# Kernel optimization log

Hardware: AMD Instinct MI355X
Metric: run time of the kernel (lower is better)

## Reference

```python
import jax, jax.numpy as jnp
import numpy as np

B, S, D, MULT, K, EPS = 8, 2048, 512, 4, 9, 1e-6


def setup_inputs() -> dict:
    key = jax.random.key(0)
    ks = jax.random.split(key, 12)
    w = lambda k, shape, s=0.02: jax.random.normal(k, shape, dtype=jnp.float32) * s
    return dict(
        x=jax.random.normal(ks[0], (B, S, D), dtype=jnp.float32),
        g=jnp.ones((D,), jnp.float32),
        W1=w(ks[1], (D, D)), b1=jnp.zeros((D,), jnp.float32),
        W2=w(ks[2], (D, D)), b2=jnp.zeros((D,), jnp.float32),
        dw_w=w(ks[3], (D, D, K)), dw_b=jnp.zeros((D,), jnp.float32),
        pw_w=w(ks[4], (D, D, 1)), pw_b=jnp.zeros((D,), jnp.float32),
        Wi=w(ks[5], (D, D)), bi=jnp.zeros((D,), jnp.float32),
        Wr=w(ks[6], (D, D)), br=jnp.zeros((D,), jnp.float32),
        lam=jax.random.normal(ks[7], (D,), dtype=jnp.float32),
        Wm1=w(ks[8], (D, D * MULT)), bm1=jnp.zeros((D * MULT,), jnp.float32),
        Wm2=w(ks[9], (D * MULT, D)), bm2=jnp.zeros((D,), jnp.float32),
    )


def _rglru(x, Wi, bi, Wr, br, lam):
    # Griffin RG-LRU: h_t = a_t * h_{t-1} + sqrt(1 - a_t^2) * (i_t * x_t), h_0 = 0
    r = jax.nn.sigmoid(x @ Wr + br)                 # [B,S,D] recurrence gate
    i = jax.nn.sigmoid(x @ Wi + bi)                 # [B,S,D] input gate
    log_a = -8.0 * jax.nn.softplus(lam) * r         # [B,S,D]
    a = jnp.exp(log_a)
    b = jnp.sqrt(1.0 - jnp.exp(2.0 * log_a)) * (i * x)

    def combine(e1, e2):
        a1, b1 = e1
        a2, b2 = e2
        return (a1 * a2, a2 * b1 + b2)

    _, h = jax.lax.associative_scan(combine, (a, b), axis=1)
    return h


def _conv1d(x_cdS, w_oik, b_o, pad):
    y = jax.lax.conv_general_dilated(
        x_cdS, w_oik, window_strides=(1,), padding=[pad],
        dimension_numbers=("NCH", "OIH", "NCH"))
    return y + b_o[None, :, None]


def reference(x, g, W1, b1, W2, b2, dw_w, dw_b, pw_w, pw_b,
              Wi, bi, Wr, br, lam, Wm1, bm1, Wm2, bm2):
    scale = jnp.sqrt(jnp.float32(D))

    def rms(t):  # matches torch: x / (||x||_2 + eps) * sqrt(D) * g
        n = jnp.linalg.norm(t, axis=-1, keepdims=True) + EPS
        return t / n * scale * g

    skip = x
    xn = rms(x)
    l1 = xn @ W1 + b1                               # [B,S,D]
    l2 = xn @ W2 + b2                               # [B,S,D]
    c = jnp.transpose(l1, (0, 2, 1))                # [B,D,S]
    c = _conv1d(c, dw_w, dw_b, (K // 2, K // 2))    # 'same' padding, k=9
    c = _conv1d(c, pw_w, pw_b, (0, 0))              # pointwise k=1
    l1 = jnp.transpose(c, (0, 2, 1))                # [B,S,D]
    l1 = _rglru(l1, Wi, bi, Wr, br, lam)
    x1 = l1 * jax.nn.gelu(l2, approximate=False) + skip

    skip2 = x1
    xn2 = rms(x1)
    h = xn2 @ Wm1 + bm1                             # [B,S,4D]
    out = (jax.nn.gelu(h, approximate=False) * h) @ Wm2 + bm2 + skip2
    return out
```

## Files before the change

kernel.cpp:

```cpp
#include <hip/hip_runtime.h>
#include <hip/hip_bf16.h>

typedef unsigned short ushort_t;
typedef unsigned short vus8 __attribute__((ext_vector_type(8)));
typedef short vs8 __attribute__((ext_vector_type(8)));
typedef float vf4 __attribute__((ext_vector_type(4)));

#define D_DIM 512
#define S_LEN 2048
#define B_SZ 8
#define T_TOK 16384
#define NCH 64
#define CLEN 32
#define APAD_ROWS 16640

__device__ __forceinline__ float bf2f(ushort_t u) {
  union { unsigned int i; float f; } v;
  v.i = ((unsigned int)u) << 16;
  return v.f;
}
__device__ __forceinline__ ushort_t f2bf(float f) {
  union { float f; unsigned int i; } v;
  v.f = f;
  unsigned int r = v.i + 0x7fffu + ((v.i >> 16) & 1u);
  return (ushort_t)(r >> 16);
}
__device__ __forceinline__ float gelu_exact(float x) {
  return 0.5f * x * (1.0f + erff(x * 0.7071067811865475f));
}
__device__ __forceinline__ float ld_in(const void* p, size_t i, int fl) {
  return fl ? ((const float*)p)[i] : bf2f(((const ushort_t*)p)[i]);
}
__device__ __forceinline__ int dt_fl(const ushort_t* gdt) {
  return !(gdt[0] == 0x3F80 && gdt[1] == 0x3F80);
}
__device__ __forceinline__ void gld_lds16(const ushort_t* g, ushort_t* l) {
  __builtin_amdgcn_global_load_lds(
      (const __attribute__((address_space(1))) unsigned int*)g,
      (__attribute__((address_space(3))) unsigned int*)l, 16, 0, 0);
}

__device__ __forceinline__ void ab_compute(ushort_t rp, ushort_t ip, ushort_t xv,
                                           float sp8, float& a, float& b) {
  float r = 1.f / (1.f + expf(-bf2f(rp)));
  float ig = 1.f / (1.f + expf(-bf2f(ip)));
  float la = -sp8 * r;
  a = expf(la);
  b = sqrtf(fmaxf(0.f, -expm1f(2.f * la))) * ig * bf2f(xv);
}

#define NJOBS 27
struct PrepJobs {
  const void* src[NJOBS];
  ushort_t* dst[NJOBS];
  int R[NJOBS];
  int C[NJOBS];
  int mode[NJOBS];
  int start[NJOBS];
  const void* gsrc;
  int njobs;
};
__global__ void mega_prep(PrepJobs J, const ushort_t* __restrict__ gdt) {
  __shared__ ushort_t ts[32][33];
  int fl = dt_fl(gdt);
  int bid = blockIdx.x;
  int j = 0;
  while (j + 1 < J.njobs && bid >= J.start[j + 1]) j++;
  int tile = bid - J.start[j];
  const void* in = J.src[j];
  ushort_t* out = J.dst[j];
  int mode = J.mode[j];
  if (mode == 2 || mode == 4) {
    int n = J.R[j];
    int base = tile * 8192;
#pragma unroll 4
    for (int q = 0; q < 32; q++) {
      int i = base + q * 256 + threadIdx.x;
      if (i < n)
        out[i] = (mode == 4) ? (ushort_t)0
                             : (fl ? f2bf(((const float*)in)[i]) : ((const ushort_t*)in)[i]);
    }
    return;
  }
  int R = J.R[j], C = J.C[j];
  int tpr = C >> 5;
  int bc = tile % tpr, br = tile / tpr;
  int tx = threadIdx.x & 31, ty = threadIdx.x >> 5;
#pragma unroll
  for (int i = 0; i < 32; i += 8) {
    size_t idx = (size_t)(br * 32 + ty + i) * C + bc * 32 + tx;
    ts[ty + i][tx] = fl ? f2bf(((const float*)in)[idx]) : ((const ushort_t*)in)[idx];
  }
  __syncthreads();
#pragma unroll
  for (int i = 0; i < 32; i += 8) {
    int r = bc * 32 + ty + i;
    int orow = (mode == 1) ? (r % 9) * 512 + r / 9 : r;
    ushort_t val = ts[tx][ty + i];
    if (mode == 3) {
      int kcol = br * 32 + tx;
      val = f2bf(bf2f(val) * ld_in(J.gsrc, kcol, fl));
    }
    out[(size_t)orow * R + br * 32 + tx] = val;
  }
}

__global__ void gam_kernel(const ushort_t* __restrict__ tpw, const ushort_t* __restrict__ dwbc,
                           const ushort_t* __restrict__ pwbc, const ushort_t* __restrict__ lamc,
                           float* __restrict__ gam, float* __restrict__ sp8b) {
  int t = blockIdx.x * 256 + threadIdx.x;
  if (t < 512) {
    float l = bf2f(lamc[t]);
    sp8b[t] = 8.f * ((l > 20.f) ? l : log1pf(expf(l)));
  }
  int wave = threadIdx.x >> 6, lane = threadIdx.x & 63;
  int o = blockIdx.x * 4 + wave;
  vus8 v = *(const vus8*)(tpw + (size_t)o * 512 + lane * 8);
  vus8 w = *(const vus8*)(dwbc + lane * 8);
  float p = 0.f;
#pragma unroll
  for (int q = 0; q < 8; q++) p += bf2f(v[q]) * bf2f(w[q]);
#pragma unroll
  for (int off = 32; off; off >>= 1) p += __shfl_xor(p, off, 64);
  if (lane == 0) gam[o] = p + bf2f(pwbc[o]);
}

__global__ void rms_kernel(const void* __restrict__ x, const ushort_t* __restrict__ gdt,
                           const ushort_t* __restrict__ gc, ushort_t* __restrict__ out) {
  int fl = dt_fl(gdt);
  int wave = threadIdx.x >> 6, lane = threadIdx.x & 63;
  int row = blockIdx.x * 4 + wave;
  size_t base = (size_t)row * D_DIM + lane * 8;
  float f[8];
  float ss = 0.f;
#pragma unroll
  for (int j = 0; j < 8; j++) { f[j] = ld_in(x, base + j, fl); ss += f[j] * f[j]; }
#pragma unroll
  for (int off = 32; off > 0; off >>= 1) ss += __shfl_xor(ss, off, 64);
  float sc = 22.62741699796952f / (sqrtf(ss) + 1e-6f);
  vus8 o;
#pragma unroll
  for (int j = 0; j < 8; j++) o[j] = f2bf(f[j] * sc * bf2f(gc[lane * 8 + j]));
  *(vus8*)(out + base) = o;
}

template <int ACT>
__global__ __launch_bounds__(256, 2) void gemm_bt(
    const ushort_t* __restrict__ A, const ushort_t* __restrict__ Bt,
    const ushort_t* __restrict__ bias, void* __restrict__ Cv,
    const ushort_t* __restrict__ skip, const float* __restrict__ rowss,
    const ushort_t* __restrict__ gdt, int N, int K, int lda, int row0,
    size_t zsA, size_t zsB, size_t zsC) {
  __shared__ __align__(16) ushort_t As[128 * 32];
  __shared__ __align__(16) ushort_t Bs[128 * 32];
  A += (size_t)blockIdx.z * zsA;
  Bt += (size_t)blockIdx.z * zsB;
  const size_t zC = (size_t)blockIdx.z * zsC;
  const int tid = threadIdx.x;
  const int bm = blockIdx.y, bn = blockIdx.x;
  const int wave = tid >> 6, lane = tid & 63;
  const int wm = wave & 1, wn = wave >> 1;
  const int quad = lane >> 4, l16 = lane & 15;
  const int ofl = (ACT == 2) ? dt_fl(gdt) : 0;
  const int srow = wave * 32 + (lane >> 2);
  const int scol = (lane & 3) * 8;
  const ushort_t* gA = A + (size_t)(bm * 128 + srow) * lda + scol;
  const ushort_t* gB = Bt + (size_t)(bn * 128 + srow) * K + scol;
  ushort_t* lA0 = As + (wave * 32) * 32;
  ushort_t* lA1 = As + (wave * 32 + 16) * 32;
  ushort_t* lB0 = Bs + (wave * 32) * 32;
  ushort_t* lB1 = Bs + (wave * 32 + 16) * 32;
  vf4 acc[4][4] = {};
  for (int k0 = 0; k0 < K; k0 += 32) {
    __syncthreads();
    gld_lds16(gA + k0, lA0);
    gld_lds16(gA + k0 + (size_t)16 * lda, lA1);
    gld_lds16(gB + k0, lB0);
    gld_lds16(gB + k0 + (size_t)16 * K, lB1);
    __syncthreads();
    vs8 af[4], bfr[4];
#pragma unroll
    for (int mi = 0; mi < 4; mi++)
      af[mi] = *(const vs8*)(As + (wm * 64 + mi * 16 + l16) * 32 + quad * 8);
#pragma unroll
    for (int ni = 0; ni < 4; ni++)
      bfr[ni] = *(const vs8*)(Bs + (wn * 64 + ni * 16 + l16) * 32 + quad * 8);
#pragma unroll
    for (int mi = 0; mi < 4; mi++)
#pragma unroll
      for (int ni = 0; ni < 4; ni++)
        acc[mi][ni] =
            __builtin_amdgcn_mfma_f32_16x16x32_bf16(af[mi], bfr[ni], acc[mi][ni], 0, 0, 0);
  }
#pragma unroll
  for (int mi = 0; mi < 4; mi++) {
#pragma unroll
    for (int ni = 0; ni < 4; ni++) {
      int gcol = bn * 128 + wn * 64 + ni * 16 + l16;
      float bv = bias ? bf2f(bias[gcol]) : 0.f;
#pragma unroll
      for (int r = 0; r < 4; r++) {
        int grow = row0 + bm * 128 + wm * 64 + mi * 16 + quad * 4 + r;
        size_t oidx = zC + (size_t)grow * N + gcol;
        float v;
        if (ACT == 3) {
          float sc = 22.62741699796952f / (sqrtf(rowss[grow]) + 1e-6f);
          v = acc[mi][ni][r] * sc + bv;
          v = gelu_exact(v) * v;
        } else {
          v = acc[mi][ni][r] + bv;
        }
        if (ACT == 2) v += bf2f(skip[(size_t)grow * N + gcol]);
        if (ACT == 2 && ofl) ((float*)Cv)[oidx] = v;
        else ((ushort_t*)Cv)[oidx] = f2bf(v);
      }
    }
  }
}

template <int ACT>
__global__ __launch_bounds__(512, 2) void gemm256(
    const ushort_t* __restrict__ A, const ushort_t* __restrict__ Bt,
    const ushort_t* __restrict__ bias, ushort_t* __restrict__ C,
    const float* __restrict__ rowss, int N, int K) {
  __shared__ __align__(16) ushort_t lds[65536];
  const int tid = threadIdx.x;
  const int bn = blockIdx.x, bm = blockIdx.y;
  const int wave = tid >> 6, lane = tid & 63;
  const int wm = wave & 1, wn = wave >> 1;
  const int quad = lane >> 4, l16 = lane & 15;
  const int NT = K >> 5;

  const int r2 = tid >> 2;
  const int scol = (((tid & 3) ^ ((r2 >> 1) & 3)) << 3);
  const ushort_t* gA0 = A + (size_t)(bm * 256 + r2) * K + scol;
  const ushort_t* gB0 = Bt + (size_t)(bn * 256 + r2) * K + scol;
  const size_t hstep = (size_t)128 * K;
  ushort_t* ldsW = lds + (wave << 9);

  const int cA = ((quad ^ ((l16 >> 1) & 3)) << 3);

  vf4 acc[8][4] = {};

#define STAGE(t, slot)                            \
  do {                                            \
    const ushort_t* ga = gA0 + (t) * 32;          \
    const ushort_t* gb = gB0 + (t) * 32;          \
    ushort_t* d = ldsW + (slot) * 16384;          \
    gld_lds16(ga, d);                             \
    gld_lds16(ga + hstep, d + 4096);              \
    gld_lds16(gb, d + 8192);                      \
    gld_lds16(gb + hstep, d + 12288);             \
  } while (0)

  STAGE(0, 0);
  STAGE(1, 1);

  for (int t = 0; t < NT; ++t) {
    if (t + 1 < NT)
      asm volatile("s_waitcnt vmcnt(4)" ::: "memory");
    else
      asm volatile("s_waitcnt vmcnt(0)" ::: "memory");
    __builtin_amdgcn_s_barrier();
    __builtin_amdgcn_sched_barrier(0);
    if (t + 2 < NT) STAGE(t + 2, (t + 2) & 3);
    const ushort_t* L = lds + (t & 3) * 16384;
    vs8 af[8], bf[4];
#pragma unroll
    for (int mi = 0; mi < 8; mi++)
      af[mi] = *(const vs8*)(L + (wm * 128 + mi * 16 + l16) * 32 + cA);
#pragma unroll
    for (int ni = 0; ni < 4; ni++)
      bf[ni] = *(const vs8*)(L + 8192 + (wn * 64 + ni * 16 + l16) * 32 + cA);
    asm volatile("s_waitcnt lgkmcnt(0)" ::: "memory");
    __builtin_amdgcn_sched_barrier(0);
    __builtin_amdgcn_s_setprio(1);
#pragma unroll
    for (int mi = 0; mi < 8; mi++)
#pragma unroll
      for (int ni = 0; ni < 4; ni++)
        acc[mi][ni] =
            __builtin_amdgcn_mfma_f32_16x16x32_bf16(af[mi], bf[ni], acc[mi][ni], 0, 0, 0);
    __builtin_amdgcn_s_setprio(0);
    __builtin_amdgcn_sched_barrier(0);
  }
#undef STAGE

#pragma unroll
  for (int mi = 0; mi < 8; mi++) {
    const int growb = bm * 256 + wm * 128 + mi * 16 + quad * 4;
    float scv[4];
    if (ACT == 3) {
#pragma unroll
      for (int r = 0; r < 4; r++)
        scv[r] = 22.62741699796952f / (sqrtf(rowss[growb + r]) + 1e-6f);
    }
#pragma unroll
    for (int ni = 0; ni < 4; ni++) {
      const int gcol = bn * 256 + wn * 64 + ni * 16 + l16;
      const float bv = bf2f(bias[gcol]);
#pragma unroll
      for (int r = 0; r < 4; r++) {
        float v = acc[mi][ni][r];
        if (ACT == 3) {
          v = v * scv[r] + bv;
          v = gelu_exact(v) * v;
        } else {
          v += bv;
        }
        int grow = growb + r;
        size_t orow = (ACT == 1) ? (size_t)grow + (size_t)((grow >> 11) << 4) + 4
                                 : (size_t)grow;
        C[orow * N + gcol] = f2bf(v);
      }
    }
  }
}

__global__ __launch_bounds__(512, 2) void conv256(
    const ushort_t* __restrict__ Apad, const ushort_t* __restrict__ Wp,
    const float* __restrict__ gam, ushort_t* __restrict__ C) {
  __shared__ __align__(16) ushort_t Asl[2 * 12288];
  __shared__ __align__(16) ushort_t Bsl[4 * 4096];
  const int tid = threadIdx.x;
  const int bn = blockIdx.x;
  const int bmg = blockIdx.y;
  const int batch = bmg >> 3, seg = bmg & 7;
  const int wave = tid >> 6, lane = tid & 63;
  const int wm = wave >> 1, wn = wave & 1;
  const int quad = lane >> 4, l16 = lane & 15;
  const int r2 = tid >> 2;
  const int sw0 = (((tid & 3) ^ ((r2 >> 1) & 3)) << 3);
  const int cB = ((quad ^ ((l16 >> 1) & 3)) << 3);
  const int bnc = bn * 128;
  const size_t tb = (size_t)batch * 2064 + seg * 256;
  const ushort_t* A0 = Apad + tb * 1024;

  vf4 acc[4][4] = {};

  auto stageA = [&](int tt, int slot, int part) {
    gld_lds16(A0 + (size_t)(part * 128 + r2) * 1024 + tt * 32 + sw0,
              Asl + slot * 12288 + part * 4096 + wave * 512);
  };
  auto stageB = [&](int tt, int pp, int slot) {
    gld_lds16(Wp + (size_t)(pp * 512 + bnc + r2) * 512 + tt * 32 + sw0,
              Bsl + slot * 4096 + wave * 512);
  };

#define CPHASE(T, P, NSTR, DO_A, DO_B)                                            \
  do {                                                                            \
    asm volatile("s_waitcnt " NSTR ::: "memory");                                 \
    __builtin_amdgcn_s_barrier();                                                 \
    __builtin_amdgcn_sched_barrier(0);                                            \
    if (DO_A) stageA((T) + 1, ((T) + 1) & 1, (P));                                \
    if (DO_B) {                                                                   \
      int pp = (P) + 2, tt = (T);                                                 \
      if (pp >= 9) { pp -= 9; tt++; }                                             \
      stageB(tt, pp, ((T) * 9 + (P) + 2) & 3);                                    \
    }                                                                             \
    const ushort_t* LA = Asl + ((T) & 1) * 12288;                                 \
    const ushort_t* LB = Bsl + (((T) * 9 + (P)) & 3) * 4096;                      \
    vs8 af[4], bfv[4];                                                            \
    _Pragma("unroll") for (int mi = 0; mi < 4; mi++) {                            \
      int row = wm * 64 + mi * 16 + l16 + (P);                                    \
      af[mi] = *(const vs8*)(LA + row * 32 + ((quad ^ ((row >> 1) & 3)) << 3));   \
    }                                                                             \
    _Pragma("unroll") for (int ni = 0; ni < 4; ni++)                              \
      bfv[ni] = *(const vs8*)(LB + (wn * 64 + ni * 16 + l16) * 32 + cB);          \
    asm volatile("s_waitcnt lgkmcnt(0)" ::: "memory");                            \
    __builtin_amdgcn_sched_barrier(0);                                            \
    __builtin_amdgcn_s_setprio(1);                                                \
    _Pragma("unroll") for (int mi = 0; mi < 4; mi++)                              \
      _Pragma("unroll") for (int ni = 0; ni < 4; ni++)                            \
        acc[mi][ni] = __builtin_amdgcn_mfma_f32_16x16x32_bf16(af[mi], bfv[ni],    \
                                                              acc[mi][ni], 0, 0, 0); \
    __builtin_amdgcn_s_setprio(0);                                                \
    __builtin_amdgcn_sched_barrier(0);                                            \
  } while (0)

  stageA(0, 0, 0);
  stageA(0, 0, 1);
  stageA(0, 0, 2);
  stageB(0, 0, 0);
  stageB(0, 1, 1);

  for (int t = 0; t < 15; ++t) {
    CPHASE(t, 0, "vmcnt(1)", 1, 1);
    CPHASE(t, 1, "vmcnt(2)", 1, 1);
    CPHASE(t, 2, "vmcnt(2)", 1, 1);
    CPHASE(t, 3, "vmcnt(2)", 0, 1);
    CPHASE(t, 4, "vmcnt(1)", 0, 1);
    CPHASE(t, 5, "vmcnt(1)", 0, 1);
    CPHASE(t, 6, "vmcnt(1)", 0, 1);
    CPHASE(t, 7, "vmcnt(1)", 0, 1);
    CPHASE(t, 8, "vmcnt(1)", 0, 1);
  }
  {
    const int t = 15;
    CPHASE(t, 0, "vmcnt(0)", 0, 1);
    CPHASE(t, 1, "vmcnt(0)", 0, 1);
    CPHASE(t, 2, "vmcnt(0)", 0, 1);
    CPHASE(t, 3, "vmcnt(0)", 0, 1);
    CPHASE(t, 4, "vmcnt(0)", 0, 1);
    CPHASE(t, 5, "vmcnt(0)", 0, 1);
    CPHASE(t, 6, "vmcnt(0)", 0, 1);
    CPHASE(t, 7, "vmcnt(0)", 0, 0);
    CPHASE(t, 8, "vmcnt(0)", 0, 0);
  }
#undef CPHASE

#pragma unroll
  for (int mi = 0; mi < 4; mi++) {
#pragma unroll
    for (int ni = 0; ni < 4; ni++) {
      int gcol = bnc + wn * 64 + ni * 16 + l16;
      float gv = gam[gcol];
#pragma unroll
      for (int r = 0; r < 4; r++) {
        int grow = (batch << 11) + seg * 256 + wm * 64 + mi * 16 + quad * 4 + r;
        C[(size_t)grow * D_DIM + gcol] = f2bf(acc[mi][ni][r] + gv);
      }
    }
  }
}

__global__ void scan_pass1(const ushort_t* __restrict__ P, const ushort_t* __restrict__ xin,
                           const float* __restrict__ sp8b, float* __restrict__ Aagg,
                           float* __restrict__ Bagg) {
  int bid = blockIdx.x;
  int dblk = bid & 1, c = (bid >> 1) & (NCH - 1), bb = bid >> 7;
  int d = dblk * 256 + threadIdx.x;
  float sp8 = sp8b[d];
  size_t baseP = ((size_t)bb * S_LEN + c * CLEN) * 1024 + d;
  size_t baseX = ((size_t)bb * S_LEN + c * CLEN) * D_DIM + d;
  float Ap = 1.f, h = 0.f;
  for (int s = 0; s < CLEN; s++) {
    float av, bv;
    ab_compute(P[baseP + (size_t)s * 1024], P[baseP + 512 + (size_t)s * 1024],
               xin[baseX + (size_t)s * D_DIM], sp8, av, bv);
    Ap *= av;
    h = av * h + bv;
  }
  size_t o = ((size_t)bb * NCH + c) * D_DIM + d;
  Aagg[o] = Ap;
  Bagg[o] = h;
}

__global__ void scan_carry(const float* __restrict__ Aagg, const float* __restrict__ Bagg,
                           float* __restrict__ carry) {
  int idx = blockIdx.x * 256 + threadIdx.x;
  int bb = idx >> 9, d = idx & (D_DIM - 1);
  float h = 0.f;
  for (int c = 0; c < NCH; c++) {
    size_t o = ((size_t)bb * NCH + c) * D_DIM + d;
    carry[o] = h;
    h = Aagg[o] * h + Bagg[o];
  }
}

__global__ void scan_pass2(const ushort_t* __restrict__ P, const float* __restrict__ sp8b,
                           const float* __restrict__ carry, const ushort_t* __restrict__ l2p,
                           const void* __restrict__ x, const ushort_t* __restrict__ gdt,
                           ushort_t* xio, float* __restrict__ rowss) {
  int fl = dt_fl(gdt);
  int bid = blockIdx.x;
  int dblk = bid & 1, c = (bid >> 1) & (NCH - 1), bb = bid >> 7;
  int d = dblk * 256 + threadIdx.x;
  int lane = threadIdx.x & 63;
  float sp8 = sp8b[d];
  float h = carry[((size_t)bb * NCH + c) * D_DIM + d];
  size_t baseP = ((size_t)bb * S_LEN + c * CLEN) * 1024 + d;
  size_t baseL = ((size_t)bb * 2064 + 4 + c * CLEN) * 1024 + 512 + d;
  size_t base = ((size_t)bb * S_LEN + c * CLEN) * D_DIM + d;
  int row0 = bb * S_LEN + c * CLEN;
  for (int s = 0; s < CLEN; s++) {
    size_t idx = base + (size_t)s * D_DIM;
    float av, bv;
    ab_compute(P[baseP + (size_t)s * 1024], P[baseP + 512 + (size_t)s * 1024], xio[idx], sp8,
               av, bv);
    h = av * h + bv;
    float l2v = bf2f(l2p[baseL + (size_t)s * 1024]);
    float xv = ld_in(x, idx, fl);
    float v = h * gelu_exact(l2v) + xv;
    xio[idx] = f2bf(v);
    float p = v * v;
#pragma unroll
    for (int o2 = 32; o2; o2 >>= 1) p += __shfl_xor(p, o2, 64);
    if (lane == 0) atomicAdd(&rowss[row0 + s], p);
  }
}

extern "C" void kernel_launch(void* const* d_in, const int* in_sizes, int n_in, void* d_out,
                              int out_size, void* d_ws, size_t ws_size, hipStream_t stream) {
  (void)in_sizes; (void)n_in; (void)out_size; (void)ws_size;
  const void* x   = d_in[0];
  const void* g   = d_in[1];
  const void* W1  = d_in[2];
  const void* b1  = d_in[3];
  const void* W2  = d_in[4];
  const void* b2  = d_in[5];
  const void* dww = d_in[6];
  const void* dwb = d_in[7];
  const void* pww = d_in[8];
  const void* pwb = d_in[9];
  const void* Wi  = d_in[10];
  const void* bi  = d_in[11];
  const void* Wr  = d_in[12];
  const void* br  = d_in[13];
  const void* lam = d_in[14];
  const void* Wm1 = d_in[15];
  const void* bm1 = d_in[16];
  const void* Wm2 = d_in[17];
  const void* bm2 = d_in[18];
  const ushort_t* gdt = (const ushort_t*)g;

  char* ws = (char*)d_ws;
  size_t off = 0;
  auto take = [&](size_t n) {
    void* p = ws + off;
    off += (n + 255) & ~(size_t)255;
    return p;
  };
  const size_t ACT_B = (size_t)T_TOK * D_DIM * 2;
  ushort_t* tW12 = (ushort_t*)take((size_t)1024 * 512 * 2);
  ushort_t* tWri = (ushort_t*)take((size_t)1024 * 512 * 2);
  ushort_t* tWm1 = (ushort_t*)take((size_t)2048 * 512 * 2);
  ushort_t* tWm2 = (ushort_t*)take((size_t)2048 * 512 * 2);
  ushort_t* Wp   = (ushort_t*)take((size_t)9 * 512 * 512 * 2);
  ushort_t* gc   = (ushort_t*)take(512 * 2);
  ushort_t* lamc = (ushort_t*)take(512 * 2);
  ushort_t* b12c = (ushort_t*)take(1024 * 2);
  ushort_t* bric = (ushort_t*)take(1024 * 2);
  ushort_t* bm2c = (ushort_t*)take(512 * 2);
  ushort_t* bm1c = (ushort_t*)take(2048 * 2);
  ushort_t* dwbc = (ushort_t*)take(512 * 2);
  ushort_t* pwbc = (ushort_t*)take(512 * 2);
  float* gam     = (float*)take(512 * 4);
  float* sp8b    = (float*)take(512 * 4);
  float* rowss   = (float*)take((size_t)T_TOK * 4);
  ushort_t* Apad2 = (ushort_t*)take((size_t)APAD_ROWS * 1024 * 2);
  ushort_t* PriB  = (ushort_t*)take((size_t)T_TOK * 1024 * 2);
  ushort_t* S4    = (ushort_t*)take(ACT_B);
  float* Aagg  = (float*)take((size_t)B_SZ * NCH * D_DIM * 4);
  float* Bagg  = (float*)take((size_t)B_SZ * NCH * D_DIM * 4);
  float* carry = (float*)take((size_t)B_SZ * NCH * D_DIM * 4);
  ushort_t* tpw  = PriB;
  ushort_t* tdwT = PriB + 262144;
  ushort_t* u    = Apad2;

  hipMemsetAsync(rowss, 0, (size_t)T_TOK * 4, stream);

  PrepJobs J;
  const void* js[NJOBS] = {g, lam, b1, b2, dwb, pwb, br, bi, bm2, bm1, pww,
                           W1, W2, Wr, Wi, Wm1, Wm2, dww,
                           nullptr, nullptr, nullptr, nullptr, nullptr, nullptr, nullptr,
                           nullptr, nullptr};
  ushort_t* jd[NJOBS] = {gc, lamc, b12c, b12c + 512, dwbc, pwbc, bric, bric + 512, bm2c, bm1c,
                         tpw, tW12, tW12 + (size_t)512 * 512, tWri, tWri + (size_t)512 * 512,
                         tWm1, tWm2, tdwT,
                         Apad2,
                         Apad2 + (size_t)(0 * 2064 + 2052) * 1024,
                         Apad2 + (size_t)(1 * 2064 + 2052) * 1024,
                         Apad2 + (size_t)(2 * 2064 + 2052) * 1024,
                         Apad2 + (size_t)(3 * 2064 + 2052) * 1024,
                         Apad2 + (size_t)(4 * 2064 + 2052) * 1024,
                         Apad2 + (size_t)(5 * 2064 + 2052) * 1024,
                         Apad2 + (size_t)(6 * 2064 + 2052) * 1024,
                         Apad2 + (size_t)(7 * 2064 + 2052) * 1024};
  int jR[NJOBS] = {512, 512, 512, 512, 512, 512, 512, 512, 512, 2048, 262144,
                   512, 512, 512, 512, 512, 2048, 512,
                   4096, 16384, 16384, 16384, 16384, 16384, 16384, 16384, 12288};
  int jC[NJOBS] = {0, 0, 0, 0, 0, 0, 0, 0, 0, 0, 0, 512, 512, 512, 512, 2048, 512, 4608,
                   0, 0, 0, 0, 0, 0, 0, 0, 0};
  int jm[NJOBS] = {2, 2, 2, 2, 2, 2, 2, 2, 2, 2, 2, 0, 0, 0, 0, 3, 0, 1,
                   4, 4, 4, 4, 4, 4, 4, 4, 4};
  int cum = 0;
  for (int i = 0; i < NJOBS; i++) {
    J.src[i] = js[i]; J.dst[i] = jd[i]; J.R[i] = jR[i]; J.C[i] = jC[i]; J.mode[i] = jm[i];
    J.start[i] = cum;
    cum += (jm[i] == 2 || jm[i] == 4) ? (jR[i] + 8191) / 8192 : (jC[i] / 32) * (jR[i] / 32);
  }
  J.gsrc = g;
  J.njobs = NJOBS;
  mega_prep<<<cum, 256, 0, stream>>>(J, gdt);
  gemm_bt<0><<<dim3(4, 4, 9), 256, 0, stream>>>(tpw, tdwT, nullptr, Wp, nullptr, nullptr, gdt,
                                                512, 512, 512, 0, 0, (size_t)512 * 512,
                                                (size_t)512 * 512);
  gam_kernel<<<128, 256, 0, stream>>>(tpw, dwbc, pwbc, lamc, gam, sp8b);

  rms_kernel<<<T_TOK / 4, 256, 0, stream>>>(x, gdt, gc, S4);
  gemm256<1><<<dim3(4, 64), 512, 0, stream>>>(S4, tW12, b12c, Apad2, nullptr, 1024, 512);
  conv256<<<dim3(4, 64), 512, 0, stream>>>(Apad2, Wp, gam, S4);
  gemm256<0><<<dim3(4, 64), 512, 0, stream>>>(S4, tWri, bric, PriB, nullptr, 1024, 512);
  scan_pass1<<<B_SZ * NCH * 2, 256, 0, stream>>>(PriB, S4, sp8b, Aagg, Bagg);
  scan_carry<<<16, 256, 0, stream>>>(Aagg, Bagg, carry);
  scan_pass2<<<B_SZ * NCH * 2, 256, 0, stream>>>(PriB, sp8b, carry, Apad2, x, gdt, S4, rowss);

  gemm256<3><<<dim3(8, 64), 512, 0, stream>>>(S4, tWm1, bm1c, u, rowss, 2048, 512);
  gemm_bt<2><<<dim3(4, 128), 256, 0, stream>>>(u, tWm2, bm2c, d_out, S4, nullptr, gdt, 512,
                                               2048, 2048, 0, 0, 0, 0);
}
```

Measured before the change: 526.9 us.

## Retile fused conv GEMM to 128x128 blocks with grouped 3-tap B staging

Replaces the 256x128-tile, 512-thread conv kernel with a 128x128-tile, 256-thread kernel launched as 512 blocks. Each phase now stages three conv taps of weights at once and reuses one A tile (128+8 rows) across all nine taps, with double buffering. Block index swizzling groups the column tiles. The aim is more blocks for occupancy and fewer barriers per K step. The cost is a full vmcnt(0) wait each phase, so loads overlap less, and more A halo is reloaded relative to the smaller tile.

```diff
diff --git a/kernel.cpp b/kernel.cpp
--- a/kernel.cpp
+++ b/kernel.cpp
@@ -317,97 +317,88 @@
   }
 }
 
-__global__ __launch_bounds__(512, 2) void conv256(
-    const ushort_t* __restrict__ Apad, const ushort_t* __restrict__ Wp,
+__global__ __launch_bounds__(256, 2) void conv_p(
+    const ushort_t* __restrict__ Apad, const ushort_t* __restrict__ Bt9,
     const float* __restrict__ gam, ushort_t* __restrict__ C) {
-  __shared__ __align__(16) ushort_t Asl[2 * 12288];
-  __shared__ __align__(16) ushort_t Bsl[4 * 4096];
+  __shared__ __align__(16) ushort_t Asl[2][4352];
+  __shared__ __align__(16) ushort_t Bsl[2][12288];
   const int tid = threadIdx.x;
-  const int bn = blockIdx.x;
-  const int bmg = blockIdx.y;
-  const int batch = bmg >> 3, seg = bmg & 7;
+  const int bid = blockIdx.x;
+  const int xid = bid & 7, cid = bid >> 3;
+  const int bn = xid >> 1;
+  const int bm = (xid & 1) * 64 + cid;
+  const int batch = bm >> 4, seg = bm & 15;
   const int wave = tid >> 6, lane = tid & 63;
-  const int wm = wave >> 1, wn = wave & 1;
+  const int wm = wave & 1, wn = wave >> 1;
   const int quad = lane >> 4, l16 = lane & 15;
-  const int r2 = tid >> 2;
-  const int sw0 = (((tid & 3) ^ ((r2 >> 1) & 3)) << 3);
+  const int lr4 = lane >> 2;
+  const int scg = (((lane & 3) ^ ((lane >> 3) & 3)) << 3);
   const int cB = ((quad ^ ((l16 >> 1) & 3)) << 3);
   const int bnc = bn * 128;
-  const size_t tb = (size_t)batch * 2064 + seg * 256;
-  const ushort_t* A0 = Apad + tb * 1024;
-
+  const size_t arow0 = (size_t)batch * 2064 + seg * 128;
+  const ushort_t* A0 = Apad + arow0 * 1024;
   vf4 acc[4][4] = {};
 
-  auto stageA = [&](int tt, int slot, int part) {
-    gld_lds16(A0 + (size_t)(part * 128 + r2) * 1024 + tt * 32 + sw0,
-              Asl + slot * 12288 + part * 4096 + wave * 512);
+  auto stageA = [&](int k0, int s) {
+    const ushort_t* src = A0 + (size_t)lr4 * 1024 + k0 * 32 + scg;
+    ushort_t* dst = &Asl[s][0];
+    gld_lds16(src + (size_t)(wave * 16) * 1024, dst + wave * 512);
+    gld_lds16(src + (size_t)(64 + wave * 16) * 1024, dst + (64 + wave * 16) * 32);
+    if (lane < 32) gld_lds16(src + (size_t)128 * 1024, dst + 128 * 32);
   };
-  auto stageB = [&](int tt, int pp, int slot) {
-    gld_lds16(Wp + (size_t)(pp * 512 + bnc + r2) * 512 + tt * 32 + sw0,
-              Bsl + slot * 4096 + wave * 512);
+  auto stageB = [&](int k0, int kg, int s) {
+#pragma unroll
+    for (int h = 0; h < 6; h++) {
+      int m = h * 4 + wave;
+      int kbl = m >> 3, r16 = m & 7;
+      const ushort_t* gsrc = Bt9 +
+          ((size_t)(kg * 3 + kbl) * D_DIM + bnc + r16 * 16 + lr4) * D_DIM + k0 * 32 + scg;
+      gld_lds16(gsrc, &Bsl[s][0] + m * 512);
+    }
   };
 
-#define CPHASE(T, P, NSTR, DO_A, DO_B)                                            \
+#define CPH(K0, KG, LASTP)                                                        \
   do {                                                                            \
-    asm volatile("s_waitcnt " NSTR ::: "memory");                                 \
+    asm volatile("s_waitcnt vmcnt(0)" ::: "memory");                              \
     __builtin_amdgcn_s_barrier();                                                 \
     __builtin_amdgcn_sched_barrier(0);                                            \
-    if (DO_A) stageA((T) + 1, ((T) + 1) & 1, (P));                                \
-    if (DO_B) {                                                                   \
-      int pp = (P) + 2, tt = (T);                                                 \
-      if (pp >= 9) { pp -= 9; tt++; }                                             \
-      stageB(tt, pp, ((T) * 9 + (P) + 2) & 3);                                    \
+    if (!(LASTP)) {                                                               \
+      int nk0 = (K0), nkg = (KG) + 1;                                             \
+      if (nkg == 3) { nkg = 0; nk0++; }                                           \
+      stageB(nk0, nkg, ((K0) * 3 + (KG) + 1) & 1);                                \
+      if ((KG) == 1 && (K0) + 1 < 16) stageA((K0) + 1, ((K0) + 1) & 1);           \
     }                                                                             \
-    const ushort_t* LA = Asl + ((T) & 1) * 12288;                                 \
-    const ushort_t* LB = Bsl + (((T) * 9 + (P)) & 3) * 4096;                      \
-    vs8 af[4], bfv[4];                                                            \
-    _Pragma("unroll") for (int mi = 0; mi < 4; mi++) {                            \
-      int row = wm * 64 + mi * 16 + l16 + (P);                                    \
-      af[mi] = *(const vs8*)(LA + row * 32 + ((quad ^ ((row >> 1) & 3)) << 3));   \
+    const ushort_t* LA = &Asl[(K0) & 1][0];                                       \
+    const ushort_t* LB = &Bsl[((K0) * 3 + (KG)) & 1][0];                          \
+    _Pragma("unroll") for (int kbl = 0; kbl < 3; kbl++) {                         \
+      int kb = (KG) * 3 + kbl;                                                    \
+      vs8 af[4], bfr[4];                                                          \
+      _Pragma("unroll") for (int mi = 0; mi < 4; mi++) {                          \
+        int row = wm * 64 + mi * 16 + l16 + kb;                                   \
+        af[mi] = *(const vs8*)(LA + row * 32 + ((quad ^ ((row >> 1) & 3)) << 3)); \
+      }                                                                           \
+      _Pragma("unroll") for (int ni = 0; ni < 4; ni++)                            \
+        bfr[ni] = *(const vs8*)(LB + kbl * 4096 + (wn * 64 + ni * 16 + l16) * 32 + cB); \
+      asm volatile("s_waitcnt lgkmcnt(0)" ::: "memory");                          \
+      __builtin_amdgcn_sched_barrier(0);                                          \
+      __builtin_amdgcn_s_setprio(1);                                              \
+      _Pragma("unroll") for (int mi = 0; mi < 4; mi++)                            \
+        _Pragma("unroll") for (int ni = 0; ni < 4; ni++)                          \
+          acc[mi][ni] = __builtin_amdgcn_mfma_f32_16x16x32_bf16(af[mi], bfr[ni],  \
+                                                                acc[mi][ni], 0, 0, 0); \
+      __builtin_amdgcn_s_setprio(0);                                              \
+      __builtin_amdgcn_sched_barrier(0);                                          \
     }                                                                             \
-    _Pragma("unroll") for (int ni = 0; ni < 4; ni++)                              \
-      bfv[ni] = *(const vs8*)(LB + (wn * 64 + ni * 16 + l16) * 32 + cB);          \
-    asm volatile("s_waitcnt lgkmcnt(0)" ::: "memory");                            \
-    __builtin_amdgcn_sched_barrier(0);                                            \
-    __builtin_amdgcn_s_setprio(1);                                                \
-    _Pragma("unroll") for (int mi = 0; mi < 4; mi++)                              \
-      _Pragma("unroll") for (int ni = 0; ni < 4; ni++)                            \
-        acc[mi][ni] = __builtin_amdgcn_mfma_f32_16x16x32_bf16(af[mi], bfv[ni],    \
-                                                              acc[mi][ni], 0, 0, 0); \
-    __builtin_amdgcn_s_setprio(0);                                                \
-    __builtin_amdgcn_sched_barrier(0);                                            \
   } while (0)
 
-  stageA(0, 0, 0);
-  stageA(0, 0, 1);
-  stageA(0, 0, 2);
+  stageA(0, 0);
   stageB(0, 0, 0);
-  stageB(0, 1, 1);
-
-  for (int t = 0; t < 15; ++t) {
-    CPHASE(t, 0, "vmcnt(1)", 1, 1);
-    CPHASE(t, 1, "vmcnt(2)", 1, 1);
-    CPHASE(t, 2, "vmcnt(2)", 1, 1);
-    CPHASE(t, 3, "vmcnt(2)", 0, 1);
-    CPHASE(t, 4, "vmcnt(1)", 0, 1);
-    CPHASE(t, 5, "vmcnt(1)", 0, 1);
-    CPHASE(t, 6, "vmcnt(1)", 0, 1);
-    CPHASE(t, 7, "vmcnt(1)", 0, 1);
-    CPHASE(t, 8, "vmcnt(1)", 0, 1);
-  }
-  {
-    const int t = 15;
-    CPHASE(t, 0, "vmcnt(0)", 0, 1);
-    CPHASE(t, 1, "vmcnt(0)", 0, 1);
-    CPHASE(t, 2, "vmcnt(0)", 0, 1);
-    CPHASE(t, 3, "vmcnt(0)", 0, 1);
-    CPHASE(t, 4, "vmcnt(0)", 0, 1);
-    CPHASE(t, 5, "vmcnt(0)", 0, 1);
-    CPHASE(t, 6, "vmcnt(0)", 0, 1);
-    CPHASE(t, 7, "vmcnt(0)", 0, 0);
-    CPHASE(t, 8, "vmcnt(0)", 0, 0);
-  }
-#undef CPHASE
+  for (int k0 = 0; k0 < 16; ++k0) {
+    CPH(k0, 0, false);
+    CPH(k0, 1, false);
+    CPH(k0, 2, k0 == 15);
+  }
+#undef CPH
 
 #pragma unroll
   for (int mi = 0; mi < 4; mi++) {
@@ -417,7 +408,7 @@
       float gv = gam[gcol];
 #pragma unroll
       for (int r = 0; r < 4; r++) {
-        int grow = (batch << 11) + seg * 256 + wm * 64 + mi * 16 + quad * 4 + r;
+        int grow = bm * 128 + wm * 64 + mi * 16 + quad * 4 + r;
         C[(size_t)grow * D_DIM + gcol] = f2bf(acc[mi][ni][r] + gv);
       }
     }
@@ -590,7 +581,7 @@
 
   rms_kernel<<<T_TOK / 4, 256, 0, stream>>>(x, gdt, gc, S4);
   gemm256<1><<<dim3(4, 64), 512, 0, stream>>>(S4, tW12, b12c, Apad2, nullptr, 1024, 512);
-  conv256<<<dim3(4, 64), 512, 0, stream>>>(Apad2, Wp, gam, S4);
+  conv_p<<<512, 256, 0, stream>>>(Apad2, Wp, gam, S4);
   gemm256<0><<<dim3(4, 64), 512, 0, stream>>>(S4, tWri, bric, PriB, nullptr, 1024, 512);
   scan_pass1<<<B_SZ * NCH * 2, 256, 0, stream>>>(PriB, S4, sp8b, Aagg, Bagg);
   scan_carry<<<16, 256, 0, stream>>>(Aagg, Bagg, carry);
```

New measurement: 503.1 us. -4.5%, faster.
